# Kernel tuning notes

Measured on AMD Instinct MI355X. Metric: run time of the kernel, lower is better.

The kernel has to match this reference:

```python
import jax, jax.numpy as jnp
import numpy as np

N_NODES = 50000


def gcn_conv(x, W, b, src, dst, n_nodes):
    """PyG GCNConv: h = x @ W; add self-loops; symmetric deg^-1/2 norm; scatter-sum; + bias."""
    h = x @ W  # [N, out]
    # degree including self-loop (edge weight 1)
    ones = jnp.ones(dst.shape[0], dtype=x.dtype)
    deg = jax.ops.segment_sum(ones, dst, num_segments=n_nodes) + 1.0  # [N]
    dinv = jax.lax.rsqrt(deg)  # deg >= 1 always (self-loop)
    # per-edge norm = dinv[src] * dinv[dst]; gather, scale, scatter-add
    msg = h[src] * (dinv[src] * dinv[dst])[:, None]  # [E, out]
    agg = jax.ops.segment_sum(msg, dst, num_segments=n_nodes)
    # self-loop contribution: norm_ii = dinv[i]^2
    agg = agg + h * (dinv * dinv)[:, None]
    return agg + b


def setup_inputs() -> dict:
    key = jax.random.key(0)
    k1, k2, k3, k4, k5 = jax.random.split(key, 5)
    in_dim, hidden_dim = 128, 128
    x = jax.random.normal(k1, (N_NODES, in_dim), dtype=jnp.float32)
    edge_index = jax.random.randint(k2, (2, 800000), 0, N_NODES, dtype=jnp.int64)
    W1 = jax.random.normal(k3, (in_dim, hidden_dim), dtype=jnp.float32) * 0.05
    b1 = jnp.zeros((hidden_dim,), dtype=jnp.float32)
    W2 = jax.random.normal(k4, (hidden_dim, 1), dtype=jnp.float32) * 0.05
    b2 = jnp.zeros((1,), dtype=jnp.float32)
    return {"x": x, "edge_index": edge_index, "W1": W1, "b1": b1, "W2": W2, "b2": b2}


def reference(x, edge_index, W1, b1, W2, b2):
    src, dst = edge_index[0], edge_index[1]
    n = x.shape[0]
    h = gcn_conv(x, W1, b1, src, dst, n)
    h = jax.nn.relu(h)  # dropout is identity in eval mode
    out = gcn_conv(h, W2, b2, src, dst, n)
    return out.squeeze(-1)  # [N]
```

## Files before the change

kernel.cpp:

```cpp
#include <hip/hip_runtime.h>
#include <hip/hip_fp16.h>

#define DIM 128
#define SCAN_TILE 2048
#define NCHK 256
#define BKT_SHIFT 8
#define BCAP 8192

typedef _Float16 half8v __attribute__((ext_vector_type(8)));
typedef float    floatx4 __attribute__((ext_vector_type(4)));

__device__ __forceinline__ void h8_to_f8(float4 raw, float* o) {
    uint4 u = __builtin_bit_cast(uint4, raw);
    float2 f0 = __half22float2(__builtin_bit_cast(__half2, u.x));
    float2 f1 = __half22float2(__builtin_bit_cast(__half2, u.y));
    float2 f2 = __half22float2(__builtin_bit_cast(__half2, u.z));
    float2 f3 = __half22float2(__builtin_bit_cast(__half2, u.w));
    o[0] = f0.x; o[1] = f0.y; o[2] = f1.x; o[3] = f1.y;
    o[4] = f2.x; o[5] = f2.y; o[6] = f3.x; o[7] = f3.y;
}
__device__ __forceinline__ void h8_acc_scaled(float4 raw, float dv, float* a) {
    float f[8];
    h8_to_f8(raw, f);
#pragma unroll
    for (int k = 0; k < 8; ++k) a[k] = fmaf(dv, f[k], a[k]);
}

__global__ __launch_bounds__(256) void init_kernel(const float* __restrict__ W,
                                                   _Float16* __restrict__ Wt,
                                                   int* __restrict__ tile_pub) {
    int i = blockIdx.x * 256 + threadIdx.x;
    if (i < 32) tile_pub[i] = 0;
    if (i < DIM * DIM) {
        int k = i >> 7, c = i & 127;
        Wt[(size_t)c * DIM + k] = (_Float16)W[i];
    }
}

__global__ __launch_bounds__(256) void k1gemm_kernel(const int* __restrict__ dst,
                                                     int E, int n, int nbkt,
                                                     unsigned short* __restrict__ rank_local,
                                                     int* __restrict__ blockhist,
                                                     const float* __restrict__ x,
                                                     const _Float16* __restrict__ Wt,
                                                     __half* __restrict__ hs) {
    const int tid = threadIdx.x;
    const int bid = blockIdx.x;
    const bool isK1 = ((bid & 3) == 0) && ((bid >> 2) < NCHK);
    if (isK1) {
        __shared__ int bhl[256];
        const int cid = bid >> 2;
        const int echk = (E + NCHK - 1) / NCHK;
        const int e0 = cid * echk, e1 = min(E, e0 + echk);
        bhl[tid] = 0;
        __syncthreads();
        for (int e = e0 + tid; e < e1; e += 256) {
            int d = min(max(dst[e], 0), n - 1);
            int r = atomicAdd(&bhl[d >> BKT_SHIFT], 1);
            rank_local[e] = (unsigned short)r;
        }
        __syncthreads();
        for (int b = tid; b < nbkt; b += 256)
            blockhist[b * NCHK + cid] = bhl[b];
        return;
    }
    const int g   = bid - 1 - min(bid >> 2, NCHK - 1);
    const int wv  = tid >> 6;
    const int l   = tid & 63;
    const int lr  = l & 15;
    const int lk  = l >> 4;
    const int brow = g * 64 + wv * 16;
    const int arow = min(brow + lr, n - 1);

    floatx4 acc[8];
#pragma unroll
    for (int ct = 0; ct < 8; ++ct) acc[ct] = (floatx4){0.f, 0.f, 0.f, 0.f};

#pragma unroll
    for (int kb = 0; kb < 4; ++kb) {
        const float* ap = x + (size_t)arow * DIM + kb * 32 + lk * 8;
        float4 a0 = ((const float4*)ap)[0];
        float4 a1 = ((const float4*)ap)[1];
        half8v af;
        af[0] = (_Float16)a0.x; af[1] = (_Float16)a0.y;
        af[2] = (_Float16)a0.z; af[3] = (_Float16)a0.w;
        af[4] = (_Float16)a1.x; af[5] = (_Float16)a1.y;
        af[6] = (_Float16)a1.z; af[7] = (_Float16)a1.w;
#pragma unroll
        for (int ct = 0; ct < 8; ++ct) {
            half8v bf = *(const half8v*)(Wt + (size_t)(ct * 16 + lr) * DIM + kb * 32 + lk * 8);
            acc[ct] = __builtin_amdgcn_mfma_f32_16x16x32_f16(af, bf, acc[ct], 0, 0, 0);
        }
    }
#pragma unroll
    for (int j = 0; j < 4; ++j) {
        int orow = brow + lk * 4 + j;
        if (orow < n) {
#pragma unroll
            for (int ct = 0; ct < 8; ++ct)
                hs[(size_t)orow * DIM + ct * 16 + lr] = __float2half(acc[ct][j]);
        }
    }
}

__global__ __launch_bounds__(256) void scan_kernel(const int* __restrict__ in,
                                                   int L, int* __restrict__ outp,
                                                   int* __restrict__ tile_pub) {
    __shared__ int s[256];
    __shared__ int bbase;
    const int t = threadIdx.x;
    const int b = blockIdx.x;
    const int base = b * SCAN_TILE + t * 8;
    int v[8];
    int tsum = 0;
#pragma unroll
    for (int k = 0; k < 8; ++k) {
        int i = base + k;
        v[k] = (i < L) ? in[i] : 0;
        tsum += v[k];
    }
    s[t] = tsum;
    if (t == 0) bbase = 0;
    __syncthreads();
#pragma unroll
    for (int off = 1; off < 256; off <<= 1) {
        int u = (t >= off) ? s[t - off] : 0;
        __syncthreads();
        s[t] += u;
        __syncthreads();
    }
    if (t == 255)
        __hip_atomic_store(&tile_pub[b], s[255] + 1, __ATOMIC_RELEASE, __HIP_MEMORY_SCOPE_AGENT);
    if (t < b) {
        int val;
        do {
            val = __hip_atomic_load(&tile_pub[t], __ATOMIC_ACQUIRE, __HIP_MEMORY_SCOPE_AGENT);
        } while (val == 0);
        atomicAdd(&bbase, val - 1);
    }
    __syncthreads();
    int run = bbase + s[t] - tsum;
#pragma unroll
    for (int k = 0; k < 8; ++k) {
        int i = base + k;
        if (i < L) outp[i] = run;
        run += v[k];
    }
}

__global__ __launch_bounds__(256) void scat_kernel(const int* __restrict__ src,
                                                   const int* __restrict__ dst,
                                                   const unsigned short* __restrict__ rank_local,
                                                   int E, int n,
                                                   const int* __restrict__ bhoff,
                                                   unsigned int* __restrict__ bedge) {
    const int cid = blockIdx.x;
    const int echk = (E + NCHK - 1) / NCHK;
    const int e0 = cid * echk, e1 = min(E, e0 + echk);
    for (int e = e0 + threadIdx.x; e < e1; e += 256) {
        int s = min(max(src[e], 0), n - 1);
        int d = min(max(dst[e], 0), n - 1);
        int bkt = d >> BKT_SHIFT;
        int pos = bhoff[bkt * NCHK + cid] + rank_local[e];
        bedge[pos] = (unsigned int)s | ((unsigned int)(d & 255) << 16);
    }
}

__global__ __launch_bounds__(256) void bcsr_kernel(const int* __restrict__ bhoff,
                                                   const unsigned int* __restrict__ bedge,
                                                   int E, int n, int nbkt,
                                                   unsigned short* __restrict__ csr,
                                                   int* __restrict__ row_off,
                                                   float* __restrict__ dinv) {
    __shared__ unsigned int ed[BCAP];
    __shared__ unsigned short rk[BCAP];
    __shared__ int h[256], s2[256], offx[256];
    const int t = threadIdx.x;
    const int g = blockIdx.x;
    const int beg = bhoff[g * NCHK];
    const int end = (g == nbkt - 1) ? E : bhoff[(g + 1) * NCHK];
    const int cntb = min(end - beg, BCAP);

    h[t] = 0;
    __syncthreads();
    for (int i = t; i < cntb; i += 256) {
        unsigned int u = bedge[beg + i];
        ed[i] = u;
        rk[i] = (unsigned short)atomicAdd(&h[(u >> 16) & 255], 1);
    }
    __syncthreads();
    int hv = h[t];
    s2[t] = hv;
    __syncthreads();
#pragma unroll
    for (int off = 1; off < 256; off <<= 1) {
        int u = (t >= off) ? s2[t - off] : 0;
        __syncthreads();
        s2[t] += u;
        __syncthreads();
    }
    offx[t] = s2[t] - hv;
    __syncthreads();
    int node = (g << BKT_SHIFT) + t;
    if (node < n) {
        row_off[node] = beg + offx[t];
        dinv[node] = rsqrtf((float)hv + 1.0f);
    }
    if (g == nbkt - 1 && t == 0) row_off[n] = E;
    for (int i = t; i < cntb; i += 256) {
        unsigned int u = ed[i];
        csr[beg + offx[(u >> 16) & 255] + rk[i]] = (unsigned short)(u & 0xFFFF);
    }
}

__global__ __launch_bounds__(256) void gather1_kernel(const int* __restrict__ row_off,
                                                      const unsigned short* __restrict__ csr,
                                                      const __half* __restrict__ hs,
                                                      const float* __restrict__ dinv,
                                                      const float* __restrict__ b1,
                                                      const float* __restrict__ W2,
                                                      float* __restrict__ ss, int n) {
    const int wave = threadIdx.x >> 6;
    const int lane = threadIdx.x & 63;
    const int node = blockIdx.x * 4 + wave;
    if (node >= n) return;

    const int rs = row_off[node];
    const int re = row_off[node + 1];
    const int q = lane & 7;
    const int g = lane >> 3;
    const float4* hs4 = (const float4*)hs;

    float a[16];
#pragma unroll
    for (int k = 0; k < 16; ++k) a[k] = 0.f;

    int j = rs + g;
    float4 r0c, r1c; float dvc;
    bool havec = (j < re);
    if (havec) {
        int s = csr[j];
        const float4* rp = hs4 + (size_t)s * 16 + 2 * q;
        r0c = rp[0]; r1c = rp[1]; dvc = dinv[s];
    }
    while (havec) {
        int jn = j + 8;
        bool haven = (jn < re);
        float4 r0n, r1n; float dvn;
        if (haven) {
            int s = csr[jn];
            const float4* rp = hs4 + (size_t)s * 16 + 2 * q;
            r0n = rp[0]; r1n = rp[1]; dvn = dinv[s];
        }
        h8_acc_scaled(r0c, dvc, a);
        h8_acc_scaled(r1c, dvc, a + 8);
        r0c = r0n; r1c = r1n; dvc = dvn;
        j = jn; havec = haven;
    }

#pragma unroll
    for (int k = 0; k < 16; ++k) {
        a[k] += __shfl_xor(a[k], 8, 64);
        a[k] += __shfl_xor(a[k], 16, 64);
        a[k] += __shfl_xor(a[k], 32, 64);
    }

    float dv = dinv[node];
    float hv[16];
    h8_to_f8(hs4[(size_t)node * 16 + 2 * q], hv);
    h8_to_f8(hs4[(size_t)node * 16 + 2 * q + 1], hv + 8);

    float bv[16], wv[16];
#pragma unroll
    for (int u = 0; u < 4; ++u) {
        float4 bq = ((const float4*)b1)[4 * q + u];
        float4 wq = ((const float4*)W2)[4 * q + u];
        bv[4 * u + 0] = bq.x; bv[4 * u + 1] = bq.y; bv[4 * u + 2] = bq.z; bv[4 * u + 3] = bq.w;
        wv[4 * u + 0] = wq.x; wv[4 * u + 1] = wq.y; wv[4 * u + 2] = wq.z; wv[4 * u + 3] = wq.w;
    }

    float p = 0.f;
#pragma unroll
    for (int k = 0; k < 16; ++k) {
        float h1 = fmaxf(fmaf(dv, fmaf(dv, hv[k], a[k]), bv[k]), 0.f);
        p = fmaf(h1, wv[k], p);
    }
    p += __shfl_xor(p, 1, 64);
    p += __shfl_xor(p, 2, 64);
    p += __shfl_xor(p, 4, 64);
    if (lane == 0) ss[node] = p * dv;
}

__global__ __launch_bounds__(256) void gather2_kernel(const int* __restrict__ row_off,
                                                      const unsigned short* __restrict__ csr,
                                                      const float* __restrict__ ss,
                                                      const float* __restrict__ dinv,
                                                      const float* __restrict__ b2,
                                                      float* __restrict__ out, int n) {
    int i = blockIdx.x * 256 + threadIdx.x;
    if (i >= n) return;
    int rs = row_off[i], re = row_off[i + 1];
    float s0 = 0.f, s1 = 0.f, s2 = 0.f, s3 = 0.f;
    int j = rs;
    for (; j + 3 < re; j += 4) {
        int c0 = csr[j], c1 = csr[j + 1], c2 = csr[j + 2], c3 = csr[j + 3];
        s0 += ss[c0]; s1 += ss[c1]; s2 += ss[c2]; s3 += ss[c3];
    }
    for (; j < re; ++j) s0 += ss[csr[j]];
    out[i] = fmaf(dinv[i], (s0 + s1) + (s2 + s3) + ss[i], b2[0]);
}

extern "C" void kernel_launch(void* const* d_in, const int* in_sizes, int n_in,
                              void* d_out, int out_size, void* d_ws, size_t ws_size,
                              hipStream_t stream) {
    const float* x   = (const float*)d_in[0];
    const int*   ei  = (const int*)d_in[1];
    const float* W1  = (const float*)d_in[2];
    const float* b1  = (const float*)d_in[3];
    const float* W2  = (const float*)d_in[4];
    const float* b2  = (const float*)d_in[5];
    float*       out = (float*)d_out;

    const int n = in_sizes[0] / DIM;
    const int E = in_sizes[1] / 2;
    const int* srcI = ei;
    const int* dstI = ei + E;
    const int nbkt = (n + 255) >> BKT_SHIFT;
    const int L = nbkt * NCHK;
    const int scan_tiles = (L + SCAN_TILE - 1) / SCAN_TILE;

    char* ws = (char*)d_ws;
    size_t off = 0;
    auto alloc = [&](size_t bytes) { void* p = ws + off; off = (off + bytes + 511) & ~(size_t)511; return p; };
    float*          dinv     = (float*)alloc((size_t)n * 4);
    int*            row_off  = (int*)  alloc((size_t)(n + 1) * 4);
    unsigned short* rank_loc = (unsigned short*)alloc((size_t)E * 2);
    int*            bhist    = (int*)  alloc((size_t)L * 4);
    int*            bhoff    = (int*)  alloc((size_t)L * 4);
    int*            tile_pub = (int*)  alloc((size_t)32 * 4);
    unsigned int*   bedge    = (unsigned int*)alloc((size_t)E * 4);
    unsigned short* csr      = (unsigned short*)alloc((size_t)E * 2);
    __half*         hs       = (__half*)alloc((size_t)n * DIM * 2);
    float*          ss       = (float*)alloc((size_t)n * 4);
    _Float16*       Wt       = (_Float16*)alloc((size_t)DIM * DIM * 2);

    const int gemm_blocks = (n + 63) / 64;

    init_kernel<<<64, 256, 0, stream>>>(W1, Wt, tile_pub);
    k1gemm_kernel<<<NCHK + gemm_blocks, 256, 0, stream>>>(dstI, E, n, nbkt, rank_loc,
                                                          bhist, x, Wt, hs);
    scan_kernel<<<scan_tiles, 256, 0, stream>>>(bhist, L, bhoff, tile_pub);
    scat_kernel<<<NCHK, 256, 0, stream>>>(srcI, dstI, rank_loc, E, n, bhoff, bedge);
    bcsr_kernel<<<nbkt, 256, 0, stream>>>(bhoff, bedge, E, n, nbkt, csr, row_off, dinv);
    gather1_kernel<<<(n + 3) / 4, 256, 0, stream>>>(row_off, csr, hs, dinv, b1, W2, ss, n);
    gather2_kernel<<<(n + 255) / 256, 256, 0, stream>>>(row_off, csr, ss, dinv, b2, out, n);
}
```

Baseline: 111.9 us.

## Split hidden features into four column planes for cache-friendly gather

The GEMM now writes the fp16 hidden matrix as four planes of 32 columns (64 bytes per node row). gather1 runs four passes, one per plane, each reading one 16-byte chunk per lane with 16 edges per wave, and writes a partial layer-2 scalar per plane into a float4 array. gather2 sums the four partials. The goal is a per-pass working set of about 3.2MB that fits in L2, so random neighbour gathers hit cache. The cost is re-reading the CSR and dinv four times, a software-pipelined prefetch loop that becomes a simple loop, and a four-times larger ss buffer.

After: 145.2 us. 29.8% more time.

```diff
diff --git a/kernel.cpp b/kernel.cpp
--- a/kernel.cpp
+++ b/kernel.cpp
@@ -97,8 +97,10 @@
         int orow = brow + lk * 4 + j;
         if (orow < n) {
 #pragma unroll
-            for (int ct = 0; ct < 8; ++ct)
-                hs[(size_t)orow * DIM + ct * 16 + lr] = __float2half(acc[ct][j]);
+            for (int ct = 0; ct < 8; ++ct) {
+                hs[((size_t)(ct >> 1) * n + orow) * 32 + (ct & 1) * 16 + lr] =
+                    __float2half(acc[ct][j]);
+            }
         }
     }
 }
@@ -219,81 +221,63 @@
                                                       const float* __restrict__ dinv,
                                                       const float* __restrict__ b1,
                                                       const float* __restrict__ W2,
-                                                      float* __restrict__ ss, int n) {
+                                                      float* __restrict__ ss4, int n,
+                                                      int blocks_per_pass) {
+    const int pass = blockIdx.x / blocks_per_pass;
+    const int pb   = blockIdx.x % blocks_per_pass;
     const int wave = threadIdx.x >> 6;
     const int lane = threadIdx.x & 63;
-    const int node = blockIdx.x * 4 + wave;
+    const int node = pb * 4 + wave;
     if (node >= n) return;
 
     const int rs = row_off[node];
     const int re = row_off[node + 1];
-    const int q = lane & 7;
-    const int g = lane >> 3;
-    const float4* hs4 = (const float4*)hs;
-
-    float a[16];
-#pragma unroll
-    for (int k = 0; k < 16; ++k) a[k] = 0.f;
-
-    int j = rs + g;
-    float4 r0c, r1c; float dvc;
-    bool havec = (j < re);
-    if (havec) {
+    const int q = lane & 3;
+    const int g = lane >> 2;
+    const float4* plane = (const float4*)hs + (size_t)pass * n * 4;
+
+    float a[8] = {0.f, 0.f, 0.f, 0.f, 0.f, 0.f, 0.f, 0.f};
+
+    for (int j = rs + g; j < re; j += 16) {
         int s = csr[j];
-        const float4* rp = hs4 + (size_t)s * 16 + 2 * q;
-        r0c = rp[0]; r1c = rp[1]; dvc = dinv[s];
-    }
-    while (havec) {
-        int jn = j + 8;
-        bool haven = (jn < re);
-        float4 r0n, r1n; float dvn;
-        if (haven) {
-            int s = csr[jn];
-            const float4* rp = hs4 + (size_t)s * 16 + 2 * q;
-            r0n = rp[0]; r1n = rp[1]; dvn = dinv[s];
-        }
-        h8_acc_scaled(r0c, dvc, a);
-        h8_acc_scaled(r1c, dvc, a + 8);
-        r0c = r0n; r1c = r1n; dvc = dvn;
-        j = jn; havec = haven;
-    }
-
-#pragma unroll
-    for (int k = 0; k < 16; ++k) {
+        float dvs = dinv[s];
+        float4 r = plane[(size_t)s * 4 + q];
+        h8_acc_scaled(r, dvs, a);
+    }
+
+#pragma unroll
+    for (int k = 0; k < 8; ++k) {
+        a[k] += __shfl_xor(a[k], 4, 64);
         a[k] += __shfl_xor(a[k], 8, 64);
         a[k] += __shfl_xor(a[k], 16, 64);
         a[k] += __shfl_xor(a[k], 32, 64);
     }
 
     float dv = dinv[node];
-    float hv[16];
-    h8_to_f8(hs4[(size_t)node * 16 + 2 * q], hv);
-    h8_to_f8(hs4[(size_t)node * 16 + 2 * q + 1], hv + 8);
-
-    float bv[16], wv[16];
-#pragma unroll
-    for (int u = 0; u < 4; ++u) {
-        float4 bq = ((const float4*)b1)[4 * q + u];
-        float4 wq = ((const float4*)W2)[4 * q + u];
-        bv[4 * u + 0] = bq.x; bv[4 * u + 1] = bq.y; bv[4 * u + 2] = bq.z; bv[4 * u + 3] = bq.w;
-        wv[4 * u + 0] = wq.x; wv[4 * u + 1] = wq.y; wv[4 * u + 2] = wq.z; wv[4 * u + 3] = wq.w;
-    }
+    float hv[8];
+    h8_to_f8(plane[(size_t)node * 4 + q], hv);
+
+    float4 bqa = ((const float4*)b1)[pass * 8 + 2 * q];
+    float4 bqb = ((const float4*)b1)[pass * 8 + 2 * q + 1];
+    float4 wqa = ((const float4*)W2)[pass * 8 + 2 * q];
+    float4 wqb = ((const float4*)W2)[pass * 8 + 2 * q + 1];
+    float bv[8] = {bqa.x, bqa.y, bqa.z, bqa.w, bqb.x, bqb.y, bqb.z, bqb.w};
+    float wv[8] = {wqa.x, wqa.y, wqa.z, wqa.w, wqb.x, wqb.y, wqb.z, wqb.w};
 
     float p = 0.f;
 #pragma unroll
-    for (int k = 0; k < 16; ++k) {
+    for (int k = 0; k < 8; ++k) {
         float h1 = fmaxf(fmaf(dv, fmaf(dv, hv[k], a[k]), bv[k]), 0.f);
         p = fmaf(h1, wv[k], p);
     }
     p += __shfl_xor(p, 1, 64);
     p += __shfl_xor(p, 2, 64);
-    p += __shfl_xor(p, 4, 64);
-    if (lane == 0) ss[node] = p * dv;
+    if (lane == 0) ss4[(size_t)node * 4 + pass] = p * dv;
 }
 
 __global__ __launch_bounds__(256) void gather2_kernel(const int* __restrict__ row_off,
                                                       const unsigned short* __restrict__ csr,
-                                                      const float* __restrict__ ss,
+                                                      const float4* __restrict__ ss4,
                                                       const float* __restrict__ dinv,
                                                       const float* __restrict__ b2,
                                                       float* __restrict__ out, int n) {
@@ -303,11 +287,22 @@
     float s0 = 0.f, s1 = 0.f, s2 = 0.f, s3 = 0.f;
     int j = rs;
     for (; j + 3 < re; j += 4) {
-        int c0 = csr[j], c1 = csr[j + 1], c2 = csr[j + 2], c3 = csr[j + 3];
-        s0 += ss[c0]; s1 += ss[c1]; s2 += ss[c2]; s3 += ss[c3];
-    }
-    for (; j < re; ++j) s0 += ss[csr[j]];
-    out[i] = fmaf(dinv[i], (s0 + s1) + (s2 + s3) + ss[i], b2[0]);
+        float4 v0 = ss4[csr[j]];
+        float4 v1 = ss4[csr[j + 1]];
+        float4 v2 = ss4[csr[j + 2]];
+        float4 v3 = ss4[csr[j + 3]];
+        s0 += (v0.x + v0.y) + (v0.z + v0.w);
+        s1 += (v1.x + v1.y) + (v1.z + v1.w);
+        s2 += (v2.x + v2.y) + (v2.z + v2.w);
+        s3 += (v3.x + v3.y) + (v3.z + v3.w);
+    }
+    for (; j < re; ++j) {
+        float4 v = ss4[csr[j]];
+        s0 += (v.x + v.y) + (v.z + v.w);
+    }
+    float4 vs = ss4[i];
+    float self = (vs.x + vs.y) + (vs.z + vs.w);
+    out[i] = fmaf(dinv[i], (s0 + s1) + (s2 + s3) + self, b2[0]);
 }
 
 extern "C" void kernel_launch(void* const* d_in, const int* in_sizes, int n_in,
@@ -341,10 +336,11 @@
     unsigned int*   bedge    = (unsigned int*)alloc((size_t)E * 4);
     unsigned short* csr      = (unsigned short*)alloc((size_t)E * 2);
     __half*         hs       = (__half*)alloc((size_t)n * DIM * 2);
-    float*          ss       = (float*)alloc((size_t)n * 4);
+    float*          ss4      = (float*)alloc((size_t)n * 4 * 4);
     _Float16*       Wt       = (_Float16*)alloc((size_t)DIM * DIM * 2);
 
     const int gemm_blocks = (n + 63) / 64;
+    const int blocks_per_pass = (n + 3) / 4;
 
     init_kernel<<<64, 256, 0, stream>>>(W1, Wt, tile_pub);
     k1gemm_kernel<<<NCHK + gemm_blocks, 256, 0, stream>>>(dstI, E, n, nbkt, rank_loc,
@@ -352,6 +348,8 @@
     scan_kernel<<<scan_tiles, 256, 0, stream>>>(bhist, L, bhoff, tile_pub);
     scat_kernel<<<NCHK, 256, 0, stream>>>(srcI, dstI, rank_loc, E, n, bhoff, bedge);
     bcsr_kernel<<<nbkt, 256, 0, stream>>>(bhoff, bedge, E, n, nbkt, csr, row_off, dinv);
-    gather1_kernel<<<(n + 3) / 4, 256, 0, stream>>>(row_off, csr, hs, dinv, b1, W2, ss, n);
-    gather2_kernel<<<(n + 255) / 256, 256, 0, stream>>>(row_off, csr, ss, dinv, b2, out, n);
-}
+    gather1_kernel<<<blocks_per_pass * 4, 256, 0, stream>>>(row_off, csr, hs, dinv, b1, W2,
+                                                            ss4, n, blocks_per_pass);
+    gather2_kernel<<<(n + 255) / 256, 256, 0, stream>>>(row_off, csr, (const float4*)ss4,
+                                                        dinv, b2, out, n);
+}
```
